# Kernel optimization log

Hardware: AMD Instinct MI355X
Metric: run time of the kernel (lower is better)

The kernel has to match this reference:

```python
import jax, jax.numpy as jnp
import numpy as np

B, N, C = 4, 1024, 1024
H = 16
HD = C // H
FF = 4 * C
EPS = 1e-6


def layernorm(x, g, b):
    mu = jnp.mean(x, axis=-1, keepdims=True)
    var = jnp.mean((x - mu) ** 2, axis=-1, keepdims=True)
    return (x - mu) * jax.lax.rsqrt(var + EPS) * g + b


def setup_inputs() -> dict:
    key = jax.random.key(0)
    ks = jax.random.split(key, 16)
    s = lambda fan_in: 1.0 / np.sqrt(fan_in)
    inp = {
        "x": jax.random.normal(ks[0], (B, N, C), dtype=jnp.float32),
        "qkv_w": jax.random.normal(ks[1], (3 * C, C), dtype=jnp.float32) * s(C),
        "qkv_b": jnp.zeros((3 * C,), jnp.float32),
        "attn_proj_w": jax.random.normal(ks[2], (C, C), dtype=jnp.float32) * s(C),
        "attn_proj_b": jnp.zeros((C,), jnp.float32),
        "blk_proj_w": jax.random.normal(ks[3], (C, C), dtype=jnp.float32) * s(C),
        "blk_proj_b": jnp.zeros((C,), jnp.float32),
        "ln1_g": jnp.ones((C,), jnp.float32),
        "ln1_b": jnp.zeros((C,), jnp.float32),
        "ln2_g": jnp.ones((C,), jnp.float32),
        "ln2_b": jnp.zeros((C,), jnp.float32),
        "fc1_w": jax.random.normal(ks[4], (FF, C), dtype=jnp.float32) * s(C),
        "fc1_b": jnp.zeros((FF,), jnp.float32),
        "fc2_w": jax.random.normal(ks[5], (C, FF), dtype=jnp.float32) * s(FF),
        "fc2_b": jnp.zeros((C,), jnp.float32),
        "mask": jnp.ones((B, N), jnp.int32),  # unused by the original forward
    }
    return inp


def reference(x, qkv_w, qkv_b, attn_proj_w, attn_proj_b, blk_proj_w, blk_proj_b,
              ln1_g, ln1_b, ln2_g, ln2_b, fc1_w, fc1_b, fc2_w, fc2_b, mask):
    shortcut = x
    xn = layernorm(x, ln1_g, ln1_b)

    # QKV projection: [B,N,3C] -> [3,B,H,N,HD]
    qkv = xn @ qkv_w.T + qkv_b
    qkv = qkv.reshape(B, N, 3, H, HD).transpose(2, 0, 3, 1, 4)
    q, k, v = qkv[0], qkv[1], qkv[2]
    scale = HD ** -0.5
    attn = jnp.einsum('bhqd,bhkd->bhqk', q * scale, k)
    attn = jax.nn.softmax(attn, axis=-1)
    o = jnp.einsum('bhqk,bhkd->bhqd', attn, v)
    o = o.transpose(0, 2, 1, 3).reshape(B, N, C)
    o = o @ attn_proj_w.T + attn_proj_b  # attention-internal proj

    x = shortcut + (o @ blk_proj_w.T + blk_proj_b)  # Block's extra proj + residual

    h = layernorm(x, ln2_g, ln2_b)
    h = jax.nn.gelu(h @ fc1_w.T + fc1_b, approximate=False)
    h = h @ fc2_w.T + fc2_b
    return x + h
```

## Files before the change

kernel.cpp:

```cpp
#include <hip/hip_runtime.h>

typedef unsigned short u16;
typedef __attribute__((ext_vector_type(8))) short short8;
typedef __attribute__((ext_vector_type(4))) float f32x4;

#define DEVI __device__ __forceinline__

static constexpr int Nn = 1024;
static constexpr int Cc = 1024;

DEVI u16 f2bf(float f) {
  union { float f; unsigned u; } v; v.f = f;
  unsigned r = v.u + 0x7fffu + ((v.u >> 16) & 1u);
  return (u16)(r >> 16);
}

DEVI void async_ld16(const void* g, void* lds) {
  __builtin_amdgcn_global_load_lds(
      (__attribute__((address_space(1))) void*)g,
      (__attribute__((address_space(3))) void*)lds, 16, 0, 0);
}

__global__ __launch_bounds__(256) void cvt_all(
    const float* __restrict__ s0, const float* __restrict__ s1,
    const float* __restrict__ s2, const float* __restrict__ s3,
    const float* __restrict__ s4, u16* __restrict__ out) {
  const size_t i = ((size_t)blockIdx.x * 256 + threadIdx.x) * 4;
  const float* src; size_t lo;
  if (i < 3145728)      { src = s0; lo = 0; }
  else if (i < 4194304) { src = s1; lo = 3145728; }
  else if (i < 5242880) { src = s2; lo = 4194304; }
  else if (i < 9437184) { src = s3; lo = 5242880; }
  else                  { src = s4; lo = 9437184; }
  const float4 v = *(const float4*)&src[i - lo];
  ushort4 o;
  o.x = f2bf(v.x); o.y = f2bf(v.y); o.z = f2bf(v.z); o.w = f2bf(v.w);
  *(ushort4*)&out[i] = o;
}

__global__ __launch_bounds__(256) void transpose_wT(const float* __restrict__ in,
                                                    u16* __restrict__ out) {
  __shared__ u16 tile[64][72];
  const int bx = blockIdx.x & 15, by = blockIdx.x >> 4;
  const int tr = threadIdx.x >> 2;
  const int tc4 = (threadIdx.x & 3) * 16;
#pragma unroll
  for (int j = 0; j < 4; ++j) {
    const float4 v = *(const float4*)&in[(size_t)(by * 64 + tr) * 1024 +
                                         bx * 64 + tc4 + j * 4];
    tile[tc4 + j * 4 + 0][tr] = f2bf(v.x);
    tile[tc4 + j * 4 + 1][tr] = f2bf(v.y);
    tile[tc4 + j * 4 + 2][tr] = f2bf(v.z);
    tile[tc4 + j * 4 + 3][tr] = f2bf(v.w);
  }
  __syncthreads();
#pragma unroll
  for (int j = 0; j < 4; ++j) {
    ushort4 o;
    o.x = tile[tr][tc4 + j * 4 + 0];
    o.y = tile[tr][tc4 + j * 4 + 1];
    o.z = tile[tr][tc4 + j * 4 + 2];
    o.w = tile[tr][tc4 + j * 4 + 3];
    *(ushort4*)&out[(size_t)(bx * 64 + tr) * 1024 + by * 64 + tc4 + j * 4] = o;
  }
}

__global__ __launch_bounds__(256) void cbias_k(const float* __restrict__ apb,
                                               const float* __restrict__ bpw,
                                               const float* __restrict__ bpb,
                                               float* __restrict__ cb) {
  const int j = blockIdx.x * 4 + (threadIdx.x >> 6);
  const int lane = threadIdx.x & 63;
  float s = 0.f;
  for (int k = lane; k < 1024; k += 64) s += apb[k] * bpw[(size_t)j * 1024 + k];
#pragma unroll
  for (int m = 1; m < 64; m <<= 1) s += __shfl_xor(s, m);
  if (lane == 0) cb[j] = s + bpb[j];
}

__global__ __launch_bounds__(256) void gemm64(const u16* __restrict__ A,
                                              const u16* __restrict__ W,
                                              u16* __restrict__ out, int K) {
  __shared__ __align__(16) u16 As[64 * 64];
  __shared__ __align__(16) u16 Bs[64 * 64];
  const int tid = threadIdx.x;
  const int wave = tid >> 6, lane = tid & 63;
  const int g = lane >> 4, lr = lane & 15;
  const int brow = (blockIdx.x >> 4) << 6, bcol = (blockIdx.x & 15) << 6;
  const int srow = lane >> 3;
  const int scg = (lane & 7) ^ srow;
  const int swz = (lr & 7) << 4;

  f32x4 acc[4];
#pragma unroll
  for (int j = 0; j < 4; ++j) acc[j] = (f32x4){0.f, 0.f, 0.f, 0.f};

  for (int k0 = 0; k0 < K; k0 += 64) {
#pragma unroll
    for (int u = 0; u < 2; ++u) {
      async_ld16(A + (size_t)(brow + u * 32 + wave * 8 + srow) * K + k0 + scg * 8,
                 (char*)As + u * 4096 + wave * 1024);
      async_ld16(W + (size_t)(bcol + u * 32 + wave * 8 + srow) * K + k0 + scg * 8,
                 (char*)Bs + u * 4096 + wave * 1024);
    }
    __syncthreads();
    short8 af[2], bf[4][2];
#pragma unroll
    for (int kk = 0; kk < 2; ++kk)
      af[kk] = *(const short8*)((char*)As + (wave * 16 + lr) * 128 +
                                ((kk * 64 + g * 16) ^ swz));
#pragma unroll
    for (int nf = 0; nf < 4; ++nf)
#pragma unroll
      for (int kk = 0; kk < 2; ++kk)
        bf[nf][kk] = *(const short8*)((char*)Bs + (nf * 16 + lr) * 128 +
                                      ((kk * 64 + g * 16) ^ swz));
#pragma unroll
    for (int nf = 0; nf < 4; ++nf)
#pragma unroll
      for (int kk = 0; kk < 2; ++kk)
        acc[nf] = __builtin_amdgcn_mfma_f32_16x16x32_bf16(af[kk], bf[nf][kk],
                                                          acc[nf], 0, 0, 0);
    __syncthreads();
  }
#pragma unroll
  for (int nf = 0; nf < 4; ++nf)
#pragma unroll
    for (int reg = 0; reg < 4; ++reg)
      out[(size_t)(brow + wave * 16 + g * 4 + reg) * 1024 +
          bcol + nf * 16 + lr] = f2bf(acc[nf][reg]);
}

__global__ __launch_bounds__(256) void vtrans(const u16* __restrict__ qkv,
                                              u16* __restrict__ vt) {
  __shared__ u16 tile[64][72];
  const int bh = blockIdx.x >> 4, tb = blockIdx.x & 15;
  const int b = bh >> 4, h = bh & 15;
  const int t0 = tb * 64;
  const int tid = threadIdx.x;
  const int rr = tid >> 3, c8 = (tid & 7) * 8;
#pragma unroll
  for (int r = 0; r < 2; ++r) {
    const int t = r * 32 + rr;
    const short8 v = *(const short8*)(qkv + (size_t)(b * Nn + t0 + t) * 3072 +
                                      2048 + h * 64 + c8);
#pragma unroll
    for (int j = 0; j < 8; ++j) tile[t][c8 + j] = (u16)v[j];
  }
  __syncthreads();
#pragma unroll
  for (int r = 0; r < 2; ++r) {
    const int d = r * 32 + rr;
    short8 o;
#pragma unroll
    for (int j = 0; j < 8; ++j) o[j] = (short)tile[c8 + j][d];
    *(short8*)(vt + (size_t)(bh * 64 + d) * 1024 + t0 + c8) = o;
  }
}

__global__ __launch_bounds__(256) void ln_bf16(const float* __restrict__ x,
                                               const float* __restrict__ gg,
                                               const float* __restrict__ bb,
                                               u16* __restrict__ out) {
  const int row = blockIdx.x;
  const float4 v = ((const float4*)(x + (size_t)row * 1024))[threadIdx.x];
  float s  = v.x + v.y + v.z + v.w;
  float s2 = v.x * v.x + v.y * v.y + v.z * v.z + v.w * v.w;
#pragma unroll
  for (int m = 1; m < 64; m <<= 1) { s += __shfl_xor(s, m); s2 += __shfl_xor(s2, m); }
  __shared__ float ps[4], ps2[4];
  const int wave = threadIdx.x >> 6;
  if ((threadIdx.x & 63) == 0) { ps[wave] = s; ps2[wave] = s2; }
  __syncthreads();
  s = ps[0] + ps[1] + ps[2] + ps[3];
  s2 = ps2[0] + ps2[1] + ps2[2] + ps2[3];
  const float mu = s * (1.0f / 1024.0f);
  const float var = s2 * (1.0f / 1024.0f) - mu * mu;
  const float rs = rsqrtf(var + 1e-6f);
  const float4 gv = ((const float4*)gg)[threadIdx.x];
  const float4 bv = ((const float4*)bb)[threadIdx.x];
  ushort4 o;
  o.x = f2bf((v.x - mu) * rs * gv.x + bv.x);
  o.y = f2bf((v.y - mu) * rs * gv.y + bv.y);
  o.z = f2bf((v.z - mu) * rs * gv.z + bv.z);
  o.w = f2bf((v.w - mu) * rs * gv.w + bv.w);
  ((ushort4*)(out + (size_t)row * 1024))[threadIdx.x] = o;
}

template <bool GELU_, bool OUTBF>
__global__ __launch_bounds__(512, 2) void gemm256(
    const u16* __restrict__ A, const u16* __restrict__ W,
    const float* __restrict__ bias, void* __restrict__ out,
    int M, int N, int K) {
  __shared__ __align__(16) u16 As[2][256 * 64];
  __shared__ __align__(16) u16 Bs[2][256 * 64];
  const int tid = threadIdx.x;
  const int wave = tid >> 6, lane = tid & 63;
  const int g = lane >> 4, lr = lane & 15;
  const int wm = wave >> 2, wn = wave & 3;
  const int ntile = N >> 8;
  const int nwg = gridDim.x;
  int bid = blockIdx.x;
  bid = (bid & 7) * (nwg >> 3) + (bid >> 3);
  const int brow = (bid / ntile) << 8, bcol = (bid % ntile) << 8;

  const int srow8 = lane >> 3;
  const int scg = (lane & 7) ^ srow8;
  const size_t aoff = (size_t)(brow + wave * 8 + srow8) * K + scg * 8;
  const size_t boff = (size_t)(bcol + wave * 8 + srow8) * K + scg * 8;
  const int ldst = wave * 1024;

  const int NT = K >> 6;

  f32x4 acc[8][4];
#pragma unroll
  for (int i = 0; i < 8; ++i)
#pragma unroll
    for (int j = 0; j < 4; ++j) acc[i][j] = (f32x4){0.f, 0.f, 0.f, 0.f};

  auto STA = [&](int s, int kt, int u) {
    async_ld16(A + aoff + (size_t)u * 64 * K + (size_t)kt * 64,
               (char*)&As[s][0] + u * 8192 + ldst);
  };
  auto STB = [&](int s, int kt, int u) {
    async_ld16(W + boff + (size_t)u * 64 * K + (size_t)kt * 64,
               (char*)&Bs[s][0] + u * 8192 + ldst);
  };

  const int aRdRow = (wm * 128 + lr) * 128;
  const int bRdRow = (wn * 64 + lr) * 128;
  const int swz = (lr & 7) << 4;

#pragma unroll
  for (int u = 0; u < 4; ++u) STB(0, 0, u);
#pragma unroll
  for (int u = 0; u < 4; ++u) STA(0, 0, u);
  asm volatile("s_waitcnt vmcnt(0)" ::: "memory");
  __builtin_amdgcn_s_barrier();

  for (int t = 0; t < NT; ++t) {
    const int c = t & 1, nc = c ^ 1;
    const int tn = (t + 1 < NT) ? t + 1 : t;
    const char* Ab = (const char*)&As[c][0];
    const char* Bb = (const char*)&Bs[c][0];

    short8 bf[4][2];
#pragma unroll
    for (int nf = 0; nf < 4; ++nf)
#pragma unroll
      for (int kk = 0; kk < 2; ++kk)
        bf[nf][kk] = *(const short8*)(Bb + bRdRow + nf * 2048 +
                                      ((kk * 64 + g * 16) ^ swz));
    short8 af[2][2];
#pragma unroll
    for (int mf = 0; mf < 2; ++mf)
#pragma unroll
      for (int kk = 0; kk < 2; ++kk)
        af[mf][kk] = *(const short8*)(Ab + aRdRow + mf * 2048 +
                                      ((kk * 64 + g * 16) ^ swz));
    STB(nc, tn, 0); STB(nc, tn, 1);
    __builtin_amdgcn_s_setprio(1);
#pragma unroll
    for (int mf = 0; mf < 2; ++mf)
#pragma unroll
      for (int nf = 0; nf < 4; ++nf)
#pragma unroll
        for (int kk = 0; kk < 2; ++kk)
          acc[mf][nf] = __builtin_amdgcn_mfma_f32_16x16x32_bf16(
              af[mf][kk], bf[nf][kk], acc[mf][nf], 0, 0, 0);
    __builtin_amdgcn_s_setprio(0);
    __builtin_amdgcn_s_barrier();

#pragma unroll
    for (int mf = 0; mf < 2; ++mf)
#pragma unroll
      for (int kk = 0; kk < 2; ++kk)
        af[mf][kk] = *(const short8*)(Ab + aRdRow + (mf + 2) * 2048 +
                                      ((kk * 64 + g * 16) ^ swz));
    STB(nc, tn, 2); STB(nc, tn, 3);
    __builtin_amdgcn_s_setprio(1);
#pragma unroll
    for (int mf = 0; mf < 2; ++mf)
#pragma unroll
      for (int nf = 0; nf < 4; ++nf)
#pragma unroll
        for (int kk = 0; kk < 2; ++kk)
          acc[mf + 2][nf] = __builtin_amdgcn_mfma_f32_16x16x32_bf16(
              af[mf][kk], bf[nf][kk], acc[mf + 2][nf], 0, 0, 0);
    __builtin_amdgcn_s_setprio(0);
    asm volatile("s_waitcnt vmcnt(4)" ::: "memory");
    __builtin_amdgcn_s_barrier();

#pragma unroll
    for (int mf = 0; mf < 2; ++mf)
#pragma unroll
      for (int kk = 0; kk < 2; ++kk)
        af[mf][kk] = *(const short8*)(Ab + aRdRow + (mf + 4) * 2048 +
                                      ((kk * 64 + g * 16) ^ swz));
    STA(nc, tn, 0); STA(nc, tn, 2);
    __builtin_amdgcn_s_setprio(1);
#pragma unroll
    for (int mf = 0; mf < 2; ++mf)
#pragma unroll
      for (int nf = 0; nf < 4; ++nf)
#pragma unroll
        for (int kk = 0; kk < 2; ++kk)
          acc[mf + 4][nf] = __builtin_amdgcn_mfma_f32_16x16x32_bf16(
              af[mf][kk], bf[nf][kk], acc[mf + 4][nf], 0, 0, 0);
    __builtin_amdgcn_s_setprio(0);
    __builtin_amdgcn_s_barrier();

#pragma unroll
    for (int mf = 0; mf < 2; ++mf)
#pragma unroll
      for (int kk = 0; kk < 2; ++kk)
        af[mf][kk] = *(const short8*)(Ab + aRdRow + (mf + 6) * 2048 +
                                      ((kk * 64 + g * 16) ^ swz));
    STA(nc, tn, 1); STA(nc, tn, 3);
    __builtin_amdgcn_s_setprio(1);
#pragma unroll
    for (int mf = 0; mf < 2; ++mf)
#pragma unroll
      for (int nf = 0; nf < 4; ++nf)
#pragma unroll
        for (int kk = 0; kk < 2; ++kk)
          acc[mf + 6][nf] = __builtin_amdgcn_mfma_f32_16x16x32_bf16(
              af[mf][kk], bf[nf][kk], acc[mf + 6][nf], 0, 0, 0);
    __builtin_amdgcn_s_setprio(0);
    asm volatile("s_waitcnt vmcnt(2)" ::: "memory");
    __builtin_amdgcn_s_barrier();
  }

#pragma unroll
  for (int mf = 0; mf < 8; ++mf)
#pragma unroll
    for (int nf = 0; nf < 4; ++nf) {
      const int cI = bcol + wn * 64 + nf * 16 + lr;
      const float bv = bias[cI];
#pragma unroll
      for (int reg = 0; reg < 4; ++reg) {
        const int r = brow + wm * 128 + mf * 16 + g * 4 + reg;
        float v = acc[mf][nf][reg] + bv;
        if (GELU_) v = 0.5f * v * (1.0f + erff(v * 0.70710678118654752f));
        if (OUTBF) ((u16*)out)[(size_t)r * N + cI] = f2bf(v);
        else       ((float*)out)[(size_t)r * N + cI] = v;
      }
    }
}

template <bool RESID, bool OUTBF>
__global__ __launch_bounds__(512, 2) void gemm128s(
    const u16* __restrict__ A, const u16* __restrict__ W,
    const float* __restrict__ bias, const float* __restrict__ resid,
    void* __restrict__ out, int M, int N, int K) {
  __shared__ __align__(16) u16 smem[32768];
  char* SA = (char*)smem;
  char* SB = SA + 32768;
  const int tid = threadIdx.x;
  const int wave = tid >> 6, lane = tid & 63;
  const int g = lane >> 4, lr = lane & 15;
  const int kg = wave & 1, ws = wave >> 1;
  const int wm = ws >> 1, wn = ws & 1;
  const int ntile = N >> 7;
  const int nwg = gridDim.x;
  int bid = blockIdx.x;
  bid = (bid & 7) * (nwg >> 3) + (bid >> 3);
  const int brow = (bid / ntile) << 7, bcol = (bid % ntile) << 7;

  const int sru = wave * 8 + (lane >> 3);
  const int scg = (lane & 7) ^ (lane >> 3);
  const int NT = K >> 6;

  f32x4 acc[4][4];
#pragma unroll
  for (int i = 0; i < 4; ++i)
#pragma unroll
    for (int j = 0; j < 4; ++j) acc[i][j] = (f32x4){0.f, 0.f, 0.f, 0.f};

  auto STA = [&](int s, int kt, int u) {
    async_ld16(A + (size_t)(brow + u * 64 + sru) * K + (size_t)kt * 64 + scg * 8,
               SA + s * 16384 + u * 8192 + wave * 1024);
  };
  auto STB = [&](int s, int kt, int u) {
    async_ld16(W + (size_t)(bcol + u * 64 + sru) * K + (size_t)kt * 64 + scg * 8,
               SB + s * 16384 + u * 8192 + wave * 1024);
  };

  const int colb = (kg * 64 + g * 16);
  const int swz = (lr & 7) << 4;

  STB(0, 0, 0); STB(0, 0, 1); STA(0, 0, 0); STA(0, 0, 1);
  asm volatile("s_waitcnt vmcnt(0)" ::: "memory");
  __builtin_amdgcn_s_barrier();

  for (int t = 0; t < NT; ++t) {
    const int c = t & 1, nc = c ^ 1;
    const int tn = (t + 1 < NT) ? t + 1 : t;
    const char* Ab = SA + c * 16384;
    const char* Bb = SB + c * 16384;

    short8 bf[4], af[2];
#pragma unroll
    for (int nf = 0; nf < 4; ++nf)
      bf[nf] = *(const short8*)(Bb + (wn * 64 + nf * 16 + lr) * 128 +
                                (colb ^ swz));
#pragma unroll
    for (int mf = 0; mf < 2; ++mf)
      af[mf] = *(const short8*)(Ab + (wm * 32 + mf * 16 + lr) * 128 +
                                (colb ^ swz));
    STB(nc, tn, 0); STB(nc, tn, 1);
    __builtin_amdgcn_s_setprio(1);
#pragma unroll
    for (int mf = 0; mf < 2; ++mf)
#pragma unroll
      for (int nf = 0; nf < 4; ++nf)
        acc[mf][nf] = __builtin_amdgcn_mfma_f32_16x16x32_bf16(
            af[mf], bf[nf], acc[mf][nf], 0, 0, 0);
    __builtin_amdgcn_s_setprio(0);
    asm volatile("s_waitcnt vmcnt(2)" ::: "memory");
    __builtin_amdgcn_s_barrier();

#pragma unroll
    for (int mf = 0; mf < 2; ++mf)
      af[mf] = *(const short8*)(Ab + (64 + wm * 32 + mf * 16 + lr) * 128 +
                                (colb ^ swz));
    STA(nc, tn, 0); STA(nc, tn, 1);
    __builtin_amdgcn_s_setprio(1);
#pragma unroll
    for (int mf = 0; mf < 2; ++mf)
#pragma unroll
      for (int nf = 0; nf < 4; ++nf)
        acc[mf + 2][nf] = __builtin_amdgcn_mfma_f32_16x16x32_bf16(
            af[mf], bf[nf], acc[mf + 2][nf], 0, 0, 0);
    __builtin_amdgcn_s_setprio(0);
    asm volatile("s_waitcnt vmcnt(1)" ::: "memory");
    __builtin_amdgcn_s_barrier();
  }

  asm volatile("s_waitcnt vmcnt(0)" ::: "memory");
  __syncthreads();
  float* pr = (float*)smem + (size_t)((wm << 1) | wn) * 4096;
  if (kg == 1) {
#pragma unroll
    for (int mf = 0; mf < 4; ++mf)
#pragma unroll
      for (int nf = 0; nf < 4; ++nf)
#pragma unroll
        for (int reg = 0; reg < 4; ++reg) {
          const int lrow = mf * 16 + g * 4 + reg;
          const int w = lrow * 64 +
                        ((nf * 16 + lr) ^ (g << 2) ^ ((g & 1) << 4));
          pr[w] = acc[mf][nf][reg];
        }
  }
  __syncthreads();
  if (kg == 0) {
#pragma unroll
    for (int mf = 0; mf < 4; ++mf) {
      const int rb = brow + ((mf < 2) ? wm * 32 + mf * 16
                                      : 64 + wm * 32 + (mf - 2) * 16);
#pragma unroll
      for (int nf = 0; nf < 4; ++nf) {
        const int cI = bcol + wn * 64 + nf * 16 + lr;
        const float bv = bias[cI];
#pragma unroll
        for (int reg = 0; reg < 4; ++reg) {
          const int lrow = mf * 16 + g * 4 + reg;
          const int w = lrow * 64 +
                        ((nf * 16 + lr) ^ (g << 2) ^ ((g & 1) << 4));
          const int r = rb + g * 4 + reg;
          float v = acc[mf][nf][reg] + pr[w] + bv;
          if (RESID) v += resid[(size_t)r * N + cI];
          if (OUTBF) ((u16*)out)[(size_t)r * N + cI] = f2bf(v);
          else       ((float*)out)[(size_t)r * N + cI] = v;
        }
      }
    }
  }
}

__global__ __launch_bounds__(256) void attn_kernel(const u16* __restrict__ qkv,
                                                   const u16* __restrict__ vt,
                                                   u16* __restrict__ o_out) {
  const int D = blockIdx.x;
  const int bh = (D & 7) + 8 * (D >> 7);
  const int qb = (D >> 3) & 15;
  const int b = bh >> 4, h = bh & 15;
  const int tid = threadIdx.x, wave = tid >> 6, lane = tid & 63;
  const int g = lane >> 4, lr = lane & 15;
  const u16* qg = qkv + (size_t)b * Nn * 3072 + h * 64;
  const u16* kg = qg + 1024;
  const u16* vgt = vt + (size_t)bh * 64 * 1024;

  __shared__ __align__(16) u16 Kl[64 * 64];
  __shared__ __align__(16) u16 Vt[64 * 64];
  __shared__ __align__(16) u16 Pl[64 * 64];

  const int q0 = qb * 64 + wave * 16;
  short8 qf[2];
#pragma unroll
  for (int kf = 0; kf < 2; ++kf)
    qf[kf] = *(const short8*)(qg + (size_t)(q0 + lr) * 3072 + kf * 32 + g * 8);

  f32x4 o[4];
  float ll[4];
#pragma unroll
  for (int df = 0; df < 4; ++df) o[df] = (f32x4){0.f, 0.f, 0.f, 0.f};
#pragma unroll
  for (int r = 0; r < 4; ++r) ll[r] = 0.f;

  for (int t0 = 0; t0 < Nn; t0 += 64) {
#pragma unroll
    for (int r = 0; r < 2; ++r) {
      const int c = r * 256 + wave * 64 + lane;
      const int t = c >> 3;
      const int ob = ((c & 7) << 4) ^ ((t & 7) << 4);
      async_ld16(kg + (size_t)(t0 + t) * 3072 + (ob >> 1),
                 (char*)Kl + (size_t)(r * 256 + wave * 64) * 16);
      async_ld16(vgt + (size_t)t * 1024 + t0 + (ob >> 1),
                 (char*)Vt + (size_t)(r * 256 + wave * 64) * 16);
    }
    __syncthreads();

    short8 kfr[4][2];
#pragma unroll
    for (int tf = 0; tf < 4; ++tf) {
      const int t = tf * 16 + lr;
#pragma unroll
      for (int kf = 0; kf < 2; ++kf)
        kfr[tf][kf] = *(const short8*)((const char*)Kl + t * 128 +
                                       ((kf * 64 + g * 16) ^ ((t & 7) << 4)));
    }
    f32x4 s[4];
    __builtin_amdgcn_s_setprio(1);
#pragma unroll
    for (int tf = 0; tf < 4; ++tf) {
      f32x4 z = (f32x4){0.f, 0.f, 0.f, 0.f};
      z = __builtin_amdgcn_mfma_f32_16x16x32_bf16(qf[0], kfr[tf][0], z, 0, 0, 0);
      z = __builtin_amdgcn_mfma_f32_16x16x32_bf16(qf[1], kfr[tf][1], z, 0, 0, 0);
      s[tf] = z;
    }
    __builtin_amdgcn_s_setprio(0);

    short8 vfr[4][2];
#pragma unroll
    for (int df = 0; df < 4; ++df) {
      const int d = df * 16 + lr;
#pragma unroll
      for (int kf = 0; kf < 2; ++kf)
        vfr[df][kf] = *(const short8*)((const char*)Vt + d * 128 +
                                       ((kf * 64 + g * 16) ^ ((d & 7) << 4)));
    }

#pragma unroll
    for (int tf = 0; tf < 4; ++tf)
#pragma unroll
      for (int reg = 0; reg < 4; ++reg) {
        const float p = __expf(s[tf][reg] * 0.125f);
        s[tf][reg] = p;
        ll[reg] += p;
      }

#pragma unroll
    for (int tf = 0; tf < 4; ++tf)
#pragma unroll
      for (int reg = 0; reg < 4; ++reg) {
        const int m = wave * 16 + g * 4 + reg;
        const int t2 = (tf * 16 + lr) * 2;
        *(u16*)((char*)Pl + m * 128 + (t2 ^ ((m & 7) << 4))) = f2bf(s[tf][reg]);
      }
    short8 pa[2];
#pragma unroll
    for (int kf = 0; kf < 2; ++kf)
      pa[kf] = *(const short8*)((const char*)Pl + (wave * 16 + lr) * 128 +
                                ((kf * 64 + g * 16) ^ ((lr & 7) << 4)));
    __builtin_amdgcn_s_setprio(1);
#pragma unroll
    for (int df = 0; df < 4; ++df) {
      o[df] = __builtin_amdgcn_mfma_f32_16x16x32_bf16(pa[0], vfr[df][0], o[df], 0, 0, 0);
      o[df] = __builtin_amdgcn_mfma_f32_16x16x32_bf16(pa[1], vfr[df][1], o[df], 0, 0, 0);
    }
    __builtin_amdgcn_s_setprio(0);
    __syncthreads();
  }

#pragma unroll
  for (int reg = 0; reg < 4; ++reg) {
#pragma unroll
    for (int msk = 1; msk < 16; msk <<= 1) ll[reg] += __shfl_xor(ll[reg], msk);
    const float inv = 1.0f / ll[reg];
    const int row = b * Nn + qb * 64 + wave * 16 + g * 4 + reg;
#pragma unroll
    for (int df = 0; df < 4; ++df) {
      const int col = h * 64 + df * 16 + lr;
      o_out[(size_t)row * 1024 + col] = f2bf(o[df][reg] * inv);
    }
  }
}

extern "C" void kernel_launch(void* const* d_in, const int* in_sizes, int n_in,
                              void* d_out, int out_size, void* d_ws, size_t ws_size,
                              hipStream_t stream) {
  const float* x    = (const float*)d_in[0];
  const float* qkvw = (const float*)d_in[1];
  const float* qkvb = (const float*)d_in[2];
  const float* apw  = (const float*)d_in[3];
  const float* apb  = (const float*)d_in[4];
  const float* bpw  = (const float*)d_in[5];
  const float* bpb  = (const float*)d_in[6];
  const float* ln1g = (const float*)d_in[7];
  const float* ln1b = (const float*)d_in[8];
  const float* ln2g = (const float*)d_in[9];
  const float* ln2b = (const float*)d_in[10];
  const float* fc1w = (const float*)d_in[11];
  const float* fc1b = (const float*)d_in[12];
  const float* fc2w = (const float*)d_in[13];
  const float* fc2b = (const float*)d_in[14];
  float* out = (float*)d_out;

  char* ws = (char*)d_ws;
  size_t off = 0;
  auto alloc = [&](size_t bytes) {
    char* p = ws + off;
    off += (bytes + 255) & ~(size_t)255;
    return p;
  };
  u16* wqkv  = (u16*)alloc((size_t)3145728 * 2);
  u16* wap   = (u16*)alloc((size_t)1048576 * 2);
  u16* wbp   = (u16*)alloc((size_t)1048576 * 2);
  u16* wfc1  = (u16*)alloc((size_t)4194304 * 2);
  u16* wfc2  = (u16*)alloc((size_t)4194304 * 2);
  u16* xn    = (u16*)alloc((size_t)4194304 * 2);
  u16* qkvbf = (u16*)alloc((size_t)12582912 * 2);
  u16* obuf  = (u16*)alloc((size_t)4194304 * 2);
  float* x2  = (float*)alloc((size_t)4194304 * 4);
  u16* wapT  = (u16*)alloc((size_t)1048576 * 2);
  u16* wc    = (u16*)alloc((size_t)1048576 * 2);
  float* cb  = (float*)alloc(1024 * 4);
  u16* vt    = (u16*)alloc((size_t)4194304 * 2);
  u16* ff    = qkvbf;
  (void)wap;

  cvt_all<<<13312, 256, 0, stream>>>(qkvw, apw, bpw, fc1w, fc2w, wqkv);
  transpose_wT<<<256, 256, 0, stream>>>(apw, wapT);
  cbias_k<<<256, 256, 0, stream>>>(apb, bpw, bpb, cb);

  gemm64<<<256, 256, 0, stream>>>(wbp, wapT, wc, 1024);

  ln_bf16<<<4096, 256, 0, stream>>>(x, ln1g, ln1b, xn);

  gemm256<false, true><<<192, 512, 0, stream>>>(
      xn, wqkv, qkvb, qkvbf, 4096, 3072, 1024);

  vtrans<<<1024, 256, 0, stream>>>(qkvbf, vt);

  attn_kernel<<<1024, 256, 0, stream>>>(qkvbf, vt, obuf);

  gemm128s<true, false><<<256, 512, 0, stream>>>(
      obuf, wc, cb, x, x2, 4096, 1024, 1024);

  ln_bf16<<<4096, 256, 0, stream>>>(x2, ln2g, ln2b, xn);

  gemm256<true, true><<<256, 512, 0, stream>>>(
      xn, wfc1, fc1b, ff, 4096, 4096, 1024);

  gemm128s<true, false><<<256, 512, 0, stream>>>(
      ff, wfc2, fc2b, x2, out, 4096, 1024, 4096);
}
```

Before: 239.3 us.

## Double-buffer attention K/V tiles and merge GEMM inner loop into two phases

The attention kernel now double-buffers the K and V tiles in LDS, issuing async loads for the next tile before computing on the current one, so global-load latency overlaps with the MFMA and softmax work. The GEMM main loop goes from four sub-phases with barriers to two, loading four A fragments at a time and issuing all B (then all A) stores per phase. This removes barriers but raises register pressure and changes how loads interleave with MFMAs. The vmcnt wait values were left as they were, which may no longer match the new count of outstanding loads.

```diff
diff --git a/kernel.cpp b/kernel.cpp
--- a/kernel.cpp
+++ b/kernel.cpp
@@ -244,24 +244,23 @@
     const char* Ab = (const char*)&As[c][0];
     const char* Bb = (const char*)&Bs[c][0];
 
-    short8 bf[4][2];
+    short8 bf[4][2], af[4][2];
 #pragma unroll
     for (int nf = 0; nf < 4; ++nf)
 #pragma unroll
       for (int kk = 0; kk < 2; ++kk)
         bf[nf][kk] = *(const short8*)(Bb + bRdRow + nf * 2048 +
                                       ((kk * 64 + g * 16) ^ swz));
-    short8 af[2][2];
-#pragma unroll
-    for (int mf = 0; mf < 2; ++mf)
+#pragma unroll
+    for (int mf = 0; mf < 4; ++mf)
 #pragma unroll
       for (int kk = 0; kk < 2; ++kk)
         af[mf][kk] = *(const short8*)(Ab + aRdRow + mf * 2048 +
                                       ((kk * 64 + g * 16) ^ swz));
-    STB(nc, tn, 0); STB(nc, tn, 1);
+    STB(nc, tn, 0); STB(nc, tn, 1); STB(nc, tn, 2); STB(nc, tn, 3);
     __builtin_amdgcn_s_setprio(1);
 #pragma unroll
-    for (int mf = 0; mf < 2; ++mf)
+    for (int mf = 0; mf < 4; ++mf)
 #pragma unroll
       for (int nf = 0; nf < 4; ++nf)
 #pragma unroll
@@ -269,63 +268,25 @@
           acc[mf][nf] = __builtin_amdgcn_mfma_f32_16x16x32_bf16(
               af[mf][kk], bf[nf][kk], acc[mf][nf], 0, 0, 0);
     __builtin_amdgcn_s_setprio(0);
-    __builtin_amdgcn_s_barrier();
-
-#pragma unroll
-    for (int mf = 0; mf < 2; ++mf)
-#pragma unroll
-      for (int kk = 0; kk < 2; ++kk)
-        af[mf][kk] = *(const short8*)(Ab + aRdRow + (mf + 2) * 2048 +
-                                      ((kk * 64 + g * 16) ^ swz));
-    STB(nc, tn, 2); STB(nc, tn, 3);
-    __builtin_amdgcn_s_setprio(1);
-#pragma unroll
-    for (int mf = 0; mf < 2; ++mf)
-#pragma unroll
-      for (int nf = 0; nf < 4; ++nf)
-#pragma unroll
-        for (int kk = 0; kk < 2; ++kk)
-          acc[mf + 2][nf] = __builtin_amdgcn_mfma_f32_16x16x32_bf16(
-              af[mf][kk], bf[nf][kk], acc[mf + 2][nf], 0, 0, 0);
-    __builtin_amdgcn_s_setprio(0);
     asm volatile("s_waitcnt vmcnt(4)" ::: "memory");
     __builtin_amdgcn_s_barrier();
 
 #pragma unroll
-    for (int mf = 0; mf < 2; ++mf)
+    for (int mf = 0; mf < 4; ++mf)
 #pragma unroll
       for (int kk = 0; kk < 2; ++kk)
         af[mf][kk] = *(const short8*)(Ab + aRdRow + (mf + 4) * 2048 +
                                       ((kk * 64 + g * 16) ^ swz));
-    STA(nc, tn, 0); STA(nc, tn, 2);
+    STA(nc, tn, 0); STA(nc, tn, 2); STA(nc, tn, 1); STA(nc, tn, 3);
     __builtin_amdgcn_s_setprio(1);
 #pragma unroll
-    for (int mf = 0; mf < 2; ++mf)
+    for (int mf = 0; mf < 4; ++mf)
 #pragma unroll
       for (int nf = 0; nf < 4; ++nf)
 #pragma unroll
         for (int kk = 0; kk < 2; ++kk)
           acc[mf + 4][nf] = __builtin_amdgcn_mfma_f32_16x16x32_bf16(
               af[mf][kk], bf[nf][kk], acc[mf + 4][nf], 0, 0, 0);
-    __builtin_amdgcn_s_setprio(0);
-    __builtin_amdgcn_s_barrier();
-
-#pragma unroll
-    for (int mf = 0; mf < 2; ++mf)
-#pragma unroll
-      for (int kk = 0; kk < 2; ++kk)
-        af[mf][kk] = *(const short8*)(Ab + aRdRow + (mf + 6) * 2048 +
-                                      ((kk * 64 + g * 16) ^ swz));
-    STA(nc, tn, 1); STA(nc, tn, 3);
-    __builtin_amdgcn_s_setprio(1);
-#pragma unroll
-    for (int mf = 0; mf < 2; ++mf)
-#pragma unroll
-      for (int nf = 0; nf < 4; ++nf)
-#pragma unroll
-        for (int kk = 0; kk < 2; ++kk)
-          acc[mf + 6][nf] = __builtin_amdgcn_mfma_f32_16x16x32_bf16(
-              af[mf][kk], bf[nf][kk], acc[mf + 6][nf], 0, 0, 0);
     __builtin_amdgcn_s_setprio(0);
     asm volatile("s_waitcnt vmcnt(2)" ::: "memory");
     __builtin_amdgcn_s_barrier();
@@ -492,8 +453,8 @@
   const u16* kg = qg + 1024;
   const u16* vgt = vt + (size_t)bh * 64 * 1024;
 
-  __shared__ __align__(16) u16 Kl[64 * 64];
-  __shared__ __align__(16) u16 Vt[64 * 64];
+  __shared__ __align__(16) u16 Kl[2][64 * 64];
+  __shared__ __align__(16) u16 Vt[2][64 * 64];
   __shared__ __align__(16) u16 Pl[64 * 64];
 
   const int q0 = qb * 64 + wave * 16;
@@ -509,18 +470,27 @@
 #pragma unroll
   for (int r = 0; r < 4; ++r) ll[r] = 0.f;
 
-  for (int t0 = 0; t0 < Nn; t0 += 64) {
+  auto stageKV = [&](int buf, int t0) {
 #pragma unroll
     for (int r = 0; r < 2; ++r) {
       const int c = r * 256 + wave * 64 + lane;
       const int t = c >> 3;
       const int ob = ((c & 7) << 4) ^ ((t & 7) << 4);
       async_ld16(kg + (size_t)(t0 + t) * 3072 + (ob >> 1),
-                 (char*)Kl + (size_t)(r * 256 + wave * 64) * 16);
+                 (char*)Kl[buf] + (size_t)(r * 256 + wave * 64) * 16);
       async_ld16(vgt + (size_t)t * 1024 + t0 + (ob >> 1),
-                 (char*)Vt + (size_t)(r * 256 + wave * 64) * 16);
-    }
-    __syncthreads();
+                 (char*)Vt[buf] + (size_t)(r * 256 + wave * 64) * 16);
+    }
+  };
+
+  stageKV(0, 0);
+  asm volatile("s_waitcnt vmcnt(0)" ::: "memory");
+  __builtin_amdgcn_s_barrier();
+
+  for (int t0 = 0; t0 < Nn; t0 += 64) {
+    const int c = (t0 >> 6) & 1, nc = c ^ 1;
+    const bool more = (t0 + 64 < Nn);
+    if (more) stageKV(nc, t0 + 64);
 
     short8 kfr[4][2];
 #pragma unroll
@@ -528,7 +498,7 @@
       const int t = tf * 16 + lr;
 #pragma unroll
       for (int kf = 0; kf < 2; ++kf)
-        kfr[tf][kf] = *(const short8*)((const char*)Kl + t * 128 +
+        kfr[tf][kf] = *(const short8*)((const char*)Kl[c] + t * 128 +
                                        ((kf * 64 + g * 16) ^ ((t & 7) << 4)));
     }
     f32x4 s[4];
@@ -548,7 +518,7 @@
       const int d = df * 16 + lr;
 #pragma unroll
       for (int kf = 0; kf < 2; ++kf)
-        vfr[df][kf] = *(const short8*)((const char*)Vt + d * 128 +
+        vfr[df][kf] = *(const short8*)((const char*)Vt[c] + d * 128 +
                                        ((kf * 64 + g * 16) ^ ((d & 7) << 4)));
     }
 
@@ -581,7 +551,11 @@
       o[df] = __builtin_amdgcn_mfma_f32_16x16x32_bf16(pa[1], vfr[df][1], o[df], 0, 0, 0);
     }
     __builtin_amdgcn_s_setprio(0);
-    __syncthreads();
+
+    if (more) {
+      asm volatile("s_waitcnt vmcnt(0)" ::: "memory");
+      __builtin_amdgcn_s_barrier();
+    }
   }
 
 #pragma unroll
```

New measurement: 248.9 us. +4.0%, slower.

## Restructure GEMM main loop into quadrant-based 4-phase MFMA schedule

Applied to the files above, without the earlier changes.

Reorganizes the inner k-tile loop of the bf16 GEMM so each phase computes a 4x2 quadrant of the 8x4 accumulator tile. A and B fragments are loaded in halves and reused across two phases, replacing the earlier pattern that reloaded 2 A fragments per phase against all 4 B fragments. It adds extra barriers, explicit lgkmcnt waits and sched_barrier fences so that LDS reads finish before the MFMAs start and loads from different waves line up. The prologue now waits with vmcnt(2) instead of draining all loads. The extra barriers could add synchronisation stalls, and holding 4 A fragments raises register pressure.

```diff
diff --git a/kernel.cpp b/kernel.cpp
--- a/kernel.cpp
+++ b/kernel.cpp
@@ -231,11 +231,9 @@
   const int bRdRow = (wn * 64 + lr) * 128;
   const int swz = (lr & 7) << 4;
 
-#pragma unroll
-  for (int u = 0; u < 4; ++u) STB(0, 0, u);
-#pragma unroll
-  for (int u = 0; u < 4; ++u) STA(0, 0, u);
-  asm volatile("s_waitcnt vmcnt(0)" ::: "memory");
+  STB(0, 0, 0); STB(0, 0, 1); STB(0, 0, 2); STB(0, 0, 3);
+  STA(0, 0, 0); STA(0, 0, 2); STA(0, 0, 1); STA(0, 0, 3);
+  asm volatile("s_waitcnt vmcnt(2)" ::: "memory");
   __builtin_amdgcn_s_barrier();
 
   for (int t = 0; t < NT; ++t) {
@@ -244,26 +242,28 @@
     const char* Ab = (const char*)&As[c][0];
     const char* Bb = (const char*)&Bs[c][0];
 
-    short8 bf[4][2];
-#pragma unroll
-    for (int nf = 0; nf < 4; ++nf)
+    short8 bf[4][2], af[4][2];
+#pragma unroll
+    for (int nf = 0; nf < 2; ++nf)
 #pragma unroll
       for (int kk = 0; kk < 2; ++kk)
         bf[nf][kk] = *(const short8*)(Bb + bRdRow + nf * 2048 +
                                       ((kk * 64 + g * 16) ^ swz));
-    short8 af[2][2];
-#pragma unroll
-    for (int mf = 0; mf < 2; ++mf)
+#pragma unroll
+    for (int mf = 0; mf < 4; ++mf)
 #pragma unroll
       for (int kk = 0; kk < 2; ++kk)
         af[mf][kk] = *(const short8*)(Ab + aRdRow + mf * 2048 +
                                       ((kk * 64 + g * 16) ^ swz));
     STB(nc, tn, 0); STB(nc, tn, 1);
-    __builtin_amdgcn_s_setprio(1);
-#pragma unroll
-    for (int mf = 0; mf < 2; ++mf)
-#pragma unroll
-      for (int nf = 0; nf < 4; ++nf)
+    __builtin_amdgcn_s_barrier();
+    asm volatile("s_waitcnt lgkmcnt(0)" ::: "memory");
+    __builtin_amdgcn_sched_barrier(0);
+    __builtin_amdgcn_s_setprio(1);
+#pragma unroll
+    for (int mf = 0; mf < 4; ++mf)
+#pragma unroll
+      for (int nf = 0; nf < 2; ++nf)
 #pragma unroll
         for (int kk = 0; kk < 2; ++kk)
           acc[mf][nf] = __builtin_amdgcn_mfma_f32_16x16x32_bf16(
@@ -272,37 +272,43 @@
     __builtin_amdgcn_s_barrier();
 
 #pragma unroll
-    for (int mf = 0; mf < 2; ++mf)
+    for (int nf = 2; nf < 4; ++nf)
 #pragma unroll
       for (int kk = 0; kk < 2; ++kk)
-        af[mf][kk] = *(const short8*)(Ab + aRdRow + (mf + 2) * 2048 +
+        bf[nf][kk] = *(const short8*)(Bb + bRdRow + nf * 2048 +
                                       ((kk * 64 + g * 16) ^ swz));
     STB(nc, tn, 2); STB(nc, tn, 3);
-    __builtin_amdgcn_s_setprio(1);
-#pragma unroll
-    for (int mf = 0; mf < 2; ++mf)
-#pragma unroll
-      for (int nf = 0; nf < 4; ++nf)
+    __builtin_amdgcn_s_barrier();
+    asm volatile("s_waitcnt lgkmcnt(0)" ::: "memory");
+    __builtin_amdgcn_sched_barrier(0);
+    __builtin_amdgcn_s_setprio(1);
+#pragma unroll
+    for (int mf = 0; mf < 4; ++mf)
+#pragma unroll
+      for (int nf = 2; nf < 4; ++nf)
 #pragma unroll
         for (int kk = 0; kk < 2; ++kk)
-          acc[mf + 2][nf] = __builtin_amdgcn_mfma_f32_16x16x32_bf16(
-              af[mf][kk], bf[nf][kk], acc[mf + 2][nf], 0, 0, 0);
+          acc[mf][nf] = __builtin_amdgcn_mfma_f32_16x16x32_bf16(
+              af[mf][kk], bf[nf][kk], acc[mf][nf], 0, 0, 0);
     __builtin_amdgcn_s_setprio(0);
     asm volatile("s_waitcnt vmcnt(4)" ::: "memory");
     __builtin_amdgcn_s_barrier();
 
 #pragma unroll
-    for (int mf = 0; mf < 2; ++mf)
+    for (int mf = 0; mf < 4; ++mf)
 #pragma unroll
       for (int kk = 0; kk < 2; ++kk)
         af[mf][kk] = *(const short8*)(Ab + aRdRow + (mf + 4) * 2048 +
                                       ((kk * 64 + g * 16) ^ swz));
     STA(nc, tn, 0); STA(nc, tn, 2);
-    __builtin_amdgcn_s_setprio(1);
-#pragma unroll
-    for (int mf = 0; mf < 2; ++mf)
-#pragma unroll
-      for (int nf = 0; nf < 4; ++nf)
+    __builtin_amdgcn_s_barrier();
+    asm volatile("s_waitcnt lgkmcnt(0)" ::: "memory");
+    __builtin_amdgcn_sched_barrier(0);
+    __builtin_amdgcn_s_setprio(1);
+#pragma unroll
+    for (int mf = 0; mf < 4; ++mf)
+#pragma unroll
+      for (int nf = 0; nf < 2; ++nf)
 #pragma unroll
         for (int kk = 0; kk < 2; ++kk)
           acc[mf + 4][nf] = __builtin_amdgcn_mfma_f32_16x16x32_bf16(
@@ -310,22 +316,17 @@
     __builtin_amdgcn_s_setprio(0);
     __builtin_amdgcn_s_barrier();
 
-#pragma unroll
-    for (int mf = 0; mf < 2; ++mf)
-#pragma unroll
-      for (int kk = 0; kk < 2; ++kk)
-        af[mf][kk] = *(const short8*)(Ab + aRdRow + (mf + 6) * 2048 +
-                                      ((kk * 64 + g * 16) ^ swz));
     STA(nc, tn, 1); STA(nc, tn, 3);
-    __builtin_amdgcn_s_setprio(1);
-#pragma unroll
-    for (int mf = 0; mf < 2; ++mf)
-#pragma unroll
-      for (int nf = 0; nf < 4; ++nf)
+    __builtin_amdgcn_s_barrier();
+    __builtin_amdgcn_s_setprio(1);
+#pragma unroll
+    for (int mf = 0; mf < 4; ++mf)
+#pragma unroll
+      for (int nf = 2; nf < 4; ++nf)
 #pragma unroll
         for (int kk = 0; kk < 2; ++kk)
-          acc[mf + 6][nf] = __builtin_amdgcn_mfma_f32_16x16x32_bf16(
-              af[mf][kk], bf[nf][kk], acc[mf + 6][nf], 0, 0, 0);
+          acc[mf + 4][nf] = __builtin_amdgcn_mfma_f32_16x16x32_bf16(
+              af[mf][kk], bf[nf][kk], acc[mf + 4][nf], 0, 0, 0);
     __builtin_amdgcn_s_setprio(0);
     asm volatile("s_waitcnt vmcnt(2)" ::: "memory");
     __builtin_amdgcn_s_barrier();
```

Result: no change. 239.6 us (+0.1%).
